# Optimization experiments

Hardware: AMD Instinct MI355X
Metric: run time of the kernel (lower is better)

## Reference

```python
import jax, jax.numpy as jnp
import numpy as np

N = 50000      # nodes
E = 800000     # edges
G = 2000       # graphs
F_IN = 34
HID = 256
H = 8
D = 32         # HID // H
L = 5


def _layer_norm(x, g, b, eps=1e-5):
    m = x.mean(-1, keepdims=True)
    v = ((x - m) ** 2).mean(-1, keepdims=True)
    return (x - m) / jnp.sqrt(v + eps) * g + b


def _gelu(x):
    return jax.nn.gelu(x, approximate=False)  # torch exact GELU


def _segment_softmax(scores, seg, n):
    # scores: [E', H], seg: [E'] target node ids
    m = jax.ops.segment_max(scores, seg, num_segments=n)
    m = jnp.where(jnp.isfinite(m), m, 0.0)
    ex = jnp.exp(scores - m[seg])
    den = jax.ops.segment_sum(ex, seg, num_segments=n)
    return ex / (den[seg] + 1e-16)


def setup_inputs() -> dict:
    key = jax.random.key(0)
    ks = iter(jax.random.split(key, 64))

    def p(shape, fan):
        return (jax.random.normal(next(ks), shape, jnp.float32) / np.sqrt(fan)).astype(jnp.float32)

    inp = {}
    inp['x'] = jax.random.normal(next(ks), (N, F_IN), jnp.float32)
    inp['edge_index'] = jax.random.randint(next(ks), (2, E), 0, N, jnp.int32)
    inp['batch'] = jnp.sort(jax.random.randint(next(ks), (N,), 0, G, jnp.int32))

    # input embed
    inp['in_W'] = p((F_IN, HID), F_IN); inp['in_b'] = jnp.zeros((HID,), jnp.float32)
    inp['in_ln_g'] = jnp.ones((HID,), jnp.float32); inp['in_ln_b'] = jnp.zeros((HID,), jnp.float32)
    # 5 GATv2 layers (stacked on leading dim)
    inp['gat_Wl'] = p((L, HID, HID), HID); inp['gat_bl'] = jnp.zeros((L, HID), jnp.float32)
    inp['gat_Wr'] = p((L, HID, HID), HID); inp['gat_br'] = jnp.zeros((L, HID), jnp.float32)
    inp['gat_att'] = p((L, H, D), D)
    inp['gat_bias'] = jnp.zeros((L, HID), jnp.float32)
    inp['gat_ln_g'] = jnp.ones((L, HID), jnp.float32); inp['gat_ln_b'] = jnp.zeros((L, HID), jnp.float32)
    # TransformerConv
    inp['tr_Wq'] = p((HID, HID), HID); inp['tr_bq'] = jnp.zeros((HID,), jnp.float32)
    inp['tr_Wk'] = p((HID, HID), HID); inp['tr_bk'] = jnp.zeros((HID,), jnp.float32)
    inp['tr_Wv'] = p((HID, HID), HID); inp['tr_bv'] = jnp.zeros((HID,), jnp.float32)
    inp['tr_Wskip'] = p((HID, HID), HID); inp['tr_bskip'] = jnp.zeros((HID,), jnp.float32)
    inp['tr_ln_g'] = jnp.ones((HID,), jnp.float32); inp['tr_ln_b'] = jnp.zeros((HID,), jnp.float32)
    # output proj
    inp['out_W'] = p((2 * HID, 2 * HID), 2 * HID); inp['out_b'] = jnp.zeros((2 * HID,), jnp.float32)
    inp['out_ln_g'] = jnp.ones((2 * HID,), jnp.float32); inp['out_ln_b'] = jnp.zeros((2 * HID,), jnp.float32)
    return inp


def reference(x, edge_index, batch,
              in_W, in_b, in_ln_g, in_ln_b,
              gat_Wl, gat_bl, gat_Wr, gat_br, gat_att, gat_bias, gat_ln_g, gat_ln_b,
              tr_Wq, tr_bq, tr_Wk, tr_bk, tr_Wv, tr_bv, tr_Wskip, tr_bskip, tr_ln_g, tr_ln_b,
              out_W, out_b, out_ln_g, out_ln_b):
    # input embedding (dropout inactive in eval)
    h = _gelu(_layer_norm(x @ in_W + in_b, in_ln_g, in_ln_b))

    src, dst = edge_index[0], edge_index[1]  # PyG: row=source j, col=target i
    loops = jnp.arange(N, dtype=src.dtype)
    s2 = jnp.concatenate([src, loops])  # GATv2 adds self loops
    d2 = jnp.concatenate([dst, loops])

    for l in range(L):  # small fixed loop over layers
        xl = (h @ gat_Wl[l] + gat_bl[l]).reshape(N, H, D)  # source transform / message
        xr = (h @ gat_Wr[l] + gat_br[l]).reshape(N, H, D)  # target transform
        e = jax.nn.leaky_relu(xl[s2] + xr[d2], 0.2)        # [E', H, D]
        score = jnp.einsum('ehd,hd->eh', e, gat_att[l])
        alpha = _segment_softmax(score, d2, N)             # softmax over incoming edges
        out = jax.ops.segment_sum(xl[s2] * alpha[..., None], d2, num_segments=N)
        out = out.reshape(N, HID) + gat_bias[l]
        h = h + _gelu(_layer_norm(out, gat_ln_g[l], gat_ln_b[l]))

    # TransformerConv (no self loops, root_weight skip connection)
    q = (h @ tr_Wq + tr_bq).reshape(N, H, D)
    k = (h @ tr_Wk + tr_bk).reshape(N, H, D)
    v = (h @ tr_Wv + tr_bv).reshape(N, H, D)
    score = (q[dst] * k[src]).sum(-1) / jnp.sqrt(jnp.float32(D))  # [E, H]
    alpha = _segment_softmax(score, dst, N)
    out = jax.ops.segment_sum(v[src] * alpha[..., None], dst, num_segments=N).reshape(N, HID)
    out = out + h @ tr_Wskip + tr_bskip
    h = h + _layer_norm(out, tr_ln_g, tr_ln_b)

    # global mean + max pool
    cnt = jax.ops.segment_sum(jnp.ones((N,), h.dtype), batch, num_segments=G)
    h_mean = jax.ops.segment_sum(h, batch, num_segments=G) / jnp.maximum(cnt, 1.0)[:, None]
    h_max = jax.ops.segment_max(h, batch, num_segments=G)
    h_max = jnp.where(jnp.isfinite(h_max), h_max, 0.0)
    ge = jnp.concatenate([h_mean, h_max], axis=-1)  # [G, 512]
    return _gelu(_layer_norm(ge @ out_W + out_b, out_ln_g, out_ln_b))
```

## Files before the change

kernel.cpp:

```cpp
#include <hip/hip_runtime.h>
#include <math.h>

#define N_NODES 50000
#define N_EDGES 800000
#define N_GRAPH 2000
#define F_INPUT 34
#define HID 256
#define NLAYER 5

typedef __attribute__((ext_vector_type(8))) short short8;
typedef __attribute__((ext_vector_type(4))) float float4v;

__device__ __forceinline__ float gelu_f(float x) {
  return 0.5f * x * (1.0f + erff(x * 0.70710678118654752440f));
}
__device__ __forceinline__ unsigned short bfr(float f) {
  unsigned u = __float_as_uint(f);
  return (unsigned short)((u + 0x7fffu + ((u >> 16) & 1u)) >> 16);
}
__device__ __forceinline__ float b2f(unsigned short s) {
  return __uint_as_float(((unsigned)s) << 16);
}
__device__ __forceinline__ float4 ld4bf(const unsigned short* p) {
  ushort4 u = *(const ushort4*)p;
  float4 f;
  f.x = b2f(u.x); f.y = b2f(u.y); f.z = b2f(u.z); f.w = b2f(u.w);
  return f;
}
__device__ __forceinline__ void unpk(unsigned u, float& a, float& b) {
  a = __uint_as_float(u << 16);
  b = __uint_as_float(u & 0xffff0000u);
}
__device__ __forceinline__ void acp16(const unsigned short* g, unsigned short* l) {
  __builtin_amdgcn_global_load_lds(
      (const __attribute__((address_space(1))) void*)g,
      (__attribute__((address_space(3))) void*)l, 16, 0, 0);
}

__global__ __launch_bounds__(256) void gemm_bias(
    const float* __restrict__ A, const float* __restrict__ B,
    const float* __restrict__ bias, float* __restrict__ C,
    int M, int Nn, int K) {
  __shared__ float As[16][64];
  __shared__ float Bs[16][64];
  int tid = threadIdx.x;
  int tx = tid & 15, ty = tid >> 4;
  int row0 = blockIdx.y * 64;
  int col0 = blockIdx.x * 64;
  float acc[4][4] = {};
  int a_r = tid >> 2;
  int a_c = (tid & 3) * 4;
  int b_r = tid >> 4;
  int b_c = (tid & 15) * 4;

  for (int k0 = 0; k0 < K; k0 += 16) {
    int ar = row0 + a_r;
#pragma unroll
    for (int i = 0; i < 4; ++i) {
      int kc = k0 + a_c + i;
      As[a_c + i][a_r] = (ar < M && kc < K) ? A[(long)ar * K + kc] : 0.f;
    }
    int bk = k0 + b_r;
    if (bk < K) {
      float4 bv = *(const float4*)&B[(long)bk * Nn + col0 + b_c];
      Bs[b_r][b_c + 0] = bv.x; Bs[b_r][b_c + 1] = bv.y;
      Bs[b_r][b_c + 2] = bv.z; Bs[b_r][b_c + 3] = bv.w;
    } else {
      Bs[b_r][b_c + 0] = 0.f; Bs[b_r][b_c + 1] = 0.f;
      Bs[b_r][b_c + 2] = 0.f; Bs[b_r][b_c + 3] = 0.f;
    }
    __syncthreads();
#pragma unroll
    for (int kk = 0; kk < 16; ++kk) {
      float4 a = *(const float4*)&As[kk][ty * 4];
      float4 b = *(const float4*)&Bs[kk][tx * 4];
      float av[4] = {a.x, a.y, a.z, a.w};
      float bv[4] = {b.x, b.y, b.z, b.w};
#pragma unroll
      for (int i = 0; i < 4; ++i)
#pragma unroll
        for (int j = 0; j < 4; ++j) acc[i][j] += av[i] * bv[j];
    }
    __syncthreads();
  }
  float4 bi = *(const float4*)&bias[col0 + tx * 4];
  float bia[4] = {bi.x, bi.y, bi.z, bi.w};
#pragma unroll
  for (int i = 0; i < 4; ++i) {
    int r = row0 + ty * 4 + i;
    if (r < M) {
      float4 o;
      o.x = acc[i][0] + bia[0]; o.y = acc[i][1] + bia[1];
      o.z = acc[i][2] + bia[2]; o.w = acc[i][3] + bia[3];
      *(float4*)&C[(long)r * Nn + col0 + tx * 4] = o;
    }
  }
}

__global__ __launch_bounds__(256) void gemm_mfma(
    const unsigned short* __restrict__ A, const unsigned short* __restrict__ Bt,
    const float* __restrict__ bias, void* __restrict__ Cv,
    int M, int Nn, int K, int flags) {
  __shared__ unsigned short smem[12288];
  unsigned short* As = smem;
  unsigned short* Bs = smem + 4096;
  int tid = threadIdx.x;
  int wave = tid >> 6, lane = tid & 63;
  int row0 = blockIdx.y * 128;
  int col0 = blockIdx.x * 128;
  int wm0 = (wave >> 1) * 64;
  int wn0 = (wave & 1) * 64;
  int q = lane >> 4;
  int ln = lane & 15;

  int srow = wave * 16 + (lane >> 2);
  int scol = (lane & 3) * 8;
  int ra0 = min(row0 + srow, M - 1);
  int ra1 = min(row0 + srow + 64, M - 1);
  const unsigned short* pa0 = A + (size_t)ra0 * K + scol;
  const unsigned short* pa1 = A + (size_t)ra1 * K + scol;
  const unsigned short* pb0 = Bt + (size_t)(col0 + srow) * K + scol;
  const unsigned short* pb1 = Bt + (size_t)(col0 + srow + 64) * K + scol;
  unsigned short* la0 = As + wave * 512;
  unsigned short* la1 = As + wave * 512 + 2048;
  unsigned short* lb0 = Bs + wave * 512;
  unsigned short* lb1 = Bs + wave * 512 + 2048;

  float4v acc[4][4];
#pragma unroll
  for (int i = 0; i < 4; ++i)
#pragma unroll
    for (int j = 0; j < 4; ++j) acc[i][j] = (float4v)0.f;

  for (int k0 = 0; k0 < K; k0 += 32) {
    acp16(pa0 + k0, la0);
    acp16(pa1 + k0, la1);
    acp16(pb0 + k0, lb0);
    acp16(pb1 + k0, lb1);
    __syncthreads();
    short8 af[4], bf[4];
#pragma unroll
    for (int i = 0; i < 4; ++i)
      af[i] = *(const short8*)&As[(wm0 + i * 16 + ln) * 32 + q * 8];
#pragma unroll
    for (int j = 0; j < 4; ++j)
      bf[j] = *(const short8*)&Bs[(wn0 + j * 16 + ln) * 32 + q * 8];
#pragma unroll
    for (int i = 0; i < 4; ++i)
#pragma unroll
      for (int j = 0; j < 4; ++j)
        acc[i][j] = __builtin_amdgcn_mfma_f32_16x16x32_bf16(af[i], bf[j], acc[i][j], 0, 0, 0);
    __syncthreads();
  }
  int rb = (lane >> 4) * 4;
  if (flags & 2) {
    unsigned short* Cb = (unsigned short*)Cv;
    unsigned short* eb = smem + wave * 2560;
#pragma unroll
    for (int p = 0; p < 2; ++p) {
#pragma unroll
      for (int jj = 0; jj < 2; ++jj) {
        int j = p * 2 + jj;
        float bv = bias[col0 + wn0 + j * 16 + ln];
#pragma unroll
        for (int i = 0; i < 4; ++i)
#pragma unroll
          for (int r = 0; r < 4; ++r)
            eb[(i * 16 + rb + r) * 40 + jj * 16 + ln] = bfr(acc[i][j][r] + bv);
      }
      int grow = row0 + wm0 + lane;
      uint4 w0 = *(uint4*)&eb[lane * 40 + 0];
      uint4 w1 = *(uint4*)&eb[lane * 40 + 8];
      uint4 w2 = *(uint4*)&eb[lane * 40 + 16];
      uint4 w3 = *(uint4*)&eb[lane * 40 + 24];
      if (grow < M) {
        unsigned short* dst = Cb + (size_t)grow * Nn + col0 + wn0 + p * 32;
        *(uint4*)&dst[0] = w0;
        *(uint4*)&dst[8] = w1;
        *(uint4*)&dst[16] = w2;
        *(uint4*)&dst[24] = w3;
      }
    }
  } else {
    float* C = (float*)Cv;
#pragma unroll
    for (int j = 0; j < 4; ++j) {
      int col = col0 + wn0 + j * 16 + ln;
      float bv = bias[col];
#pragma unroll
      for (int i = 0; i < 4; ++i)
#pragma unroll
        for (int r = 0; r < 4; ++r) {
          int row = row0 + wm0 + i * 16 + rb + r;
          if (row < M) C[(size_t)row * Nn + col] = acc[i][j][r] + bv;
        }
    }
  }
}

__global__ __launch_bounds__(256) void prep_w(
    const float* __restrict__ Wl, const float* __restrict__ Wr,
    const float* __restrict__ Wq, const float* __restrict__ Wk,
    const float* __restrict__ Wv, const float* __restrict__ Wsk,
    unsigned short* __restrict__ out) {
  __shared__ float t[32][33];
  int m = blockIdx.z;
  const float* W = (m < 10) ? (((m & 1) ? Wr : Wl) + (size_t)(m >> 1) * 65536)
                 : (m == 10) ? Wq : (m == 11) ? Wk : (m == 12) ? Wv : Wsk;
  int k0 = blockIdx.y * 32, n0 = blockIdx.x * 32;
  int r = threadIdx.x >> 5, c = threadIdx.x & 31;
  for (int rr = r; rr < 32; rr += 8)
    t[rr][c] = W[(size_t)(k0 + rr) * HID + n0 + c];
  __syncthreads();
  for (int rr = r; rr < 32; rr += 8) {
    int n = n0 + rr;
    unsigned short* o;
    int drow;
    if (m == 11) {
      o = out + (size_t)10 * 65536;
      drow = 256 + (n >> 2) * 8 + (n & 3);
    } else if (m == 12) {
      o = out + (size_t)10 * 65536;
      drow = 256 + (n >> 2) * 8 + 4 + (n & 3);
    } else {
      o = out + (size_t)m * 65536;
      drow = n;
    }
    o[(size_t)drow * HID + k0 + c] = bfr(t[c][rr]);
  }
}

__global__ __launch_bounds__(256) void prep_wout(const float* __restrict__ W,
                                                 unsigned short* __restrict__ o) {
  __shared__ float t[32][33];
  int k0 = blockIdx.y * 32, n0 = blockIdx.x * 32;
  int r = threadIdx.x >> 5, c = threadIdx.x & 31;
  for (int rr = r; rr < 32; rr += 8)
    t[rr][c] = W[(size_t)(k0 + rr) * 512 + n0 + c];
  __syncthreads();
  for (int rr = r; rr < 32; rr += 8)
    o[(size_t)(n0 + rr) * 512 + k0 + c] = bfr(t[c][rr]);
}

__global__ __launch_bounds__(256) void prep_bias(
    const float* __restrict__ bl, const float* __restrict__ br,
    const float* __restrict__ bq, const float* __restrict__ bk,
    const float* __restrict__ bv, float* __restrict__ out) {
  int i = blockIdx.x * 256 + threadIdx.x;
  if (i < 2560) {
    int l = i >> 9, c = i & 511;
    out[i] = (c < 256) ? bl[l * 256 + c] : br[l * 256 + (c - 256)];
  } else if (i < 3328) {
    int j = i - 2560;
    if (j < 256) {
      out[i] = bq[j];
    } else {
      int t = j - 256, g = t >> 3, r = t & 7;
      out[i] = (r < 4) ? bk[4 * g + r] : bv[4 * g + (r - 4)];
    }
  }
}

__global__ __launch_bounds__(256) void ln_act(
    const float* __restrict__ in, const float* __restrict__ gam,
    const float* __restrict__ bet, float* __restrict__ out,
    unsigned short* __restrict__ outb,
    int n_rows, int width, int do_gelu) {
  int wid = blockIdx.x * 4 + (threadIdx.x >> 6);
  int lane = threadIdx.x & 63;
  if (wid >= n_rows) return;
  int chunks = width >> 8;
  float4 v[2];
  float s = 0.f;
  for (int c = 0; c < chunks; ++c) {
    int off = c * 256 + lane * 4;
    float4 t = *(const float4*)&in[(size_t)wid * width + off];
    v[c] = t;
    s += t.x + t.y + t.z + t.w;
  }
  for (int o = 1; o < 64; o <<= 1) s += __shfl_xor(s, o);
  float mean = s / (float)width;
  float vs = 0.f;
  for (int c = 0; c < chunks; ++c) {
    float dx = v[c].x - mean, dy = v[c].y - mean, dz = v[c].z - mean, dw = v[c].w - mean;
    vs += dx * dx + dy * dy + dz * dz + dw * dw;
  }
  for (int o = 1; o < 64; o <<= 1) vs += __shfl_xor(vs, o);
  float inv = rsqrtf(vs / (float)width + 1e-5f);
  for (int c = 0; c < chunks; ++c) {
    int off = c * 256 + lane * 4;
    float4 g4 = *(const float4*)&gam[off];
    float4 b4 = *(const float4*)&bet[off];
    float y[4] = {(v[c].x - mean) * inv * g4.x + b4.x,
                  (v[c].y - mean) * inv * g4.y + b4.y,
                  (v[c].z - mean) * inv * g4.z + b4.z,
                  (v[c].w - mean) * inv * g4.w + b4.w};
    if (do_gelu) {
#pragma unroll
      for (int i = 0; i < 4; ++i) y[i] = gelu_f(y[i]);
    }
    size_t idx = (size_t)wid * width + off;
    float4 o4 = {y[0], y[1], y[2], y[3]};
    *(float4*)&out[idx] = o4;
    if (outb) {
      ushort4 ob = {bfr(y[0]), bfr(y[1]), bfr(y[2]), bfr(y[3])};
      *(ushort4*)&outb[idx] = ob;
    }
  }
}

__global__ __launch_bounds__(256) void edge_count(const int* __restrict__ ei,
                                                  int* __restrict__ counts) {
  int e = blockIdx.x * 256 + threadIdx.x;
  if (e < N_EDGES) atomicAdd(&counts[ei[N_EDGES + e]], 1);
}

__global__ __launch_bounds__(1024) void scan1(const int* __restrict__ counts,
                                              int* __restrict__ indptr,
                                              int* __restrict__ bsums, int n) {
  __shared__ int sm[1024];
  int tid = threadIdx.x;
  int i = blockIdx.x * 1024 + tid;
  int v = (i < n) ? counts[i] : 0;
  sm[tid] = v;
  __syncthreads();
  for (int off = 1; off < 1024; off <<= 1) {
    int t = (tid >= off) ? sm[tid - off] : 0;
    __syncthreads();
    sm[tid] += t;
    __syncthreads();
  }
  if (i < n) indptr[i] = sm[tid] - v;
  if (tid == 1023) bsums[blockIdx.x] = sm[1023];
}

__global__ __launch_bounds__(256) void scan3(const int* __restrict__ bsums,
                                             int* __restrict__ indptr,
                                             int* __restrict__ cursor, int n) {
  int i = blockIdx.x * 256 + threadIdx.x;
  int blk = blockIdx.x >> 2;
  int off = 0;
  for (int b = 0; b < blk; ++b) off += bsums[b];
  if (i < n) {
    int v = indptr[i] + off;
    indptr[i] = v;
    cursor[i] = v;
  }
  if (i == 0) indptr[n] = N_EDGES;
}

__global__ __launch_bounds__(256) void edge_scatter(const int* __restrict__ ei,
                                                    int* __restrict__ cursor,
                                                    int* __restrict__ esrc) {
  int e = blockIdx.x * 256 + threadIdx.x;
  if (e < N_EDGES) {
    int d = ei[N_EDGES + e];
    int p = atomicAdd(&cursor[d], 1);
    esrc[p] = ei[e];
  }
}

#define GAT_EDGE(f)                                                        \
  {                                                                        \
    float ex = f.x + xri.x; ex = ex > 0.f ? ex : 0.2f * ex;                \
    float ey = f.y + xri.y; ey = ey > 0.f ? ey : 0.2f * ey;                \
    float ez = f.z + xri.z; ez = ez > 0.f ? ez : 0.2f * ez;                \
    float ew = f.w + xri.w; ew = ew > 0.f ? ew : 0.2f * ew;                \
    float p = ex * a4.x + ey * a4.y + ez * a4.z + ew * a4.w;               \
    p += __shfl_xor(p, 1); p += __shfl_xor(p, 2); p += __shfl_xor(p, 4);   \
    float wgt = __expf(fminf(p - m0, 60.f));                               \
    ax += wgt * f.x; ay += wgt * f.y; az += wgt * f.z; aw += wgt * f.w;    \
    lsum += wgt;                                                           \
  }

__global__ __launch_bounds__(256) void gat_agg(
    const unsigned short* __restrict__ xlr, const float* __restrict__ att,
    const int* __restrict__ indptr, const int* __restrict__ esrc,
    const float* __restrict__ pre_bias, const float* __restrict__ gam,
    const float* __restrict__ bet, float* __restrict__ h,
    unsigned short* __restrict__ hb) {
  int wid = blockIdx.x * 4 + (threadIdx.x >> 6);
  int lane = threadIdx.x & 63;
  if (wid >= N_NODES) return;
  float4 xri = ld4bf(&xlr[(size_t)wid * 512 + 256 + lane * 4]);
  float4 a4 = *(const float4*)&att[lane * 4];
  int beg = indptr[wid], end = indptr[wid + 1];

  float m0, lsum, ax, ay, az, aw;
  {
    float4 f = ld4bf(&xlr[(size_t)wid * 512 + lane * 4]);
    float ex = f.x + xri.x; ex = ex > 0.f ? ex : 0.2f * ex;
    float ey = f.y + xri.y; ey = ey > 0.f ? ey : 0.2f * ey;
    float ez = f.z + xri.z; ez = ez > 0.f ? ez : 0.2f * ez;
    float ew = f.w + xri.w; ew = ew > 0.f ? ew : 0.2f * ew;
    float p = ex * a4.x + ey * a4.y + ez * a4.z + ew * a4.w;
    p += __shfl_xor(p, 1); p += __shfl_xor(p, 2); p += __shfl_xor(p, 4);
    m0 = p; lsum = 1.f;
    ax = f.x; ay = f.y; az = f.z; aw = f.w;
  }
  int e = beg;
  for (; e + 7 < end; e += 8) {
    int j0 = esrc[e],     j1 = esrc[e + 1], j2 = esrc[e + 2], j3 = esrc[e + 3];
    int j4 = esrc[e + 4], j5 = esrc[e + 5], j6 = esrc[e + 6], j7 = esrc[e + 7];
    float4 f0 = ld4bf(&xlr[(size_t)j0 * 512 + lane * 4]);
    float4 f1 = ld4bf(&xlr[(size_t)j1 * 512 + lane * 4]);
    float4 f2 = ld4bf(&xlr[(size_t)j2 * 512 + lane * 4]);
    float4 f3 = ld4bf(&xlr[(size_t)j3 * 512 + lane * 4]);
    float4 f4 = ld4bf(&xlr[(size_t)j4 * 512 + lane * 4]);
    float4 f5 = ld4bf(&xlr[(size_t)j5 * 512 + lane * 4]);
    float4 f6 = ld4bf(&xlr[(size_t)j6 * 512 + lane * 4]);
    float4 f7 = ld4bf(&xlr[(size_t)j7 * 512 + lane * 4]);
    GAT_EDGE(f0); GAT_EDGE(f1); GAT_EDGE(f2); GAT_EDGE(f3);
    GAT_EDGE(f4); GAT_EDGE(f5); GAT_EDGE(f6); GAT_EDGE(f7);
  }
  for (; e + 3 < end; e += 4) {
    int j0 = esrc[e], j1 = esrc[e + 1], j2 = esrc[e + 2], j3 = esrc[e + 3];
    float4 f0 = ld4bf(&xlr[(size_t)j0 * 512 + lane * 4]);
    float4 f1 = ld4bf(&xlr[(size_t)j1 * 512 + lane * 4]);
    float4 f2 = ld4bf(&xlr[(size_t)j2 * 512 + lane * 4]);
    float4 f3 = ld4bf(&xlr[(size_t)j3 * 512 + lane * 4]);
    GAT_EDGE(f0); GAT_EDGE(f1); GAT_EDGE(f2); GAT_EDGE(f3);
  }
  for (; e < end; ++e) {
    int j = esrc[e];
    float4 f = ld4bf(&xlr[(size_t)j * 512 + lane * 4]);
    GAT_EDGE(f);
  }
  float inv = 1.f / (lsum + 1e-16f);
  float4 pb = *(const float4*)&pre_bias[lane * 4];
  float y0 = ax * inv + pb.x, y1 = ay * inv + pb.y;
  float y2 = az * inv + pb.z, y3 = aw * inv + pb.w;
  float s = y0 + y1 + y2 + y3;
  for (int o = 1; o < 64; o <<= 1) s += __shfl_xor(s, o);
  float mean = s * (1.f / 256.f);
  float d0 = y0 - mean, d1 = y1 - mean, d2 = y2 - mean, d3 = y3 - mean;
  float vs = d0 * d0 + d1 * d1 + d2 * d2 + d3 * d3;
  for (int o = 1; o < 64; o <<= 1) vs += __shfl_xor(vs, o);
  float inv2 = rsqrtf(vs * (1.f / 256.f) + 1e-5f);
  float4 g4 = *(const float4*)&gam[lane * 4];
  float4 b4 = *(const float4*)&bet[lane * 4];
  size_t idx = (size_t)wid * HID + lane * 4;
  float4 r4 = *(const float4*)&h[idx];
  y0 = gelu_f(d0 * inv2 * g4.x + b4.x) + r4.x;
  y1 = gelu_f(d1 * inv2 * g4.y + b4.y) + r4.y;
  y2 = gelu_f(d2 * inv2 * g4.z + b4.z) + r4.z;
  y3 = gelu_f(d3 * inv2 * g4.w + b4.w) + r4.w;
  float4 o4 = {y0, y1, y2, y3};
  *(float4*)&h[idx] = o4;
  ushort4 ob = {bfr(y0), bfr(y1), bfr(y2), bfr(y3)};
  *(ushort4*)&hb[idx] = ob;
}

#define TR_EDGE_I(u)                                                       \
  {                                                                        \
    float kx, ky, kz, kw, vx, vy, vz, vw;                                  \
    unpk(u.x, kx, ky); unpk(u.y, kz, kw);                                  \
    unpk(u.z, vx, vy); unpk(u.w, vz, vw);                                  \
    float p = qi.x * kx + qi.y * ky + qi.z * kz + qi.w * kw;               \
    p += __shfl_xor(p, 1); p += __shfl_xor(p, 2); p += __shfl_xor(p, 4);   \
    float wgt = __expf(fminf(p * scale, 60.f));                            \
    ax += wgt * vx; ay += wgt * vy; az += wgt * vz; aw += wgt * vw;        \
    lsum += wgt;                                                           \
  }

__global__ __launch_bounds__(256) void tr_agg(
    const unsigned short* __restrict__ qkv, const int* __restrict__ indptr,
    const int* __restrict__ esrc, const unsigned short* __restrict__ skipb,
    const float* __restrict__ gam, const float* __restrict__ bet,
    float* __restrict__ h) {
  __shared__ float comb[2][5][64];
  int tid = threadIdx.x;
  int wave = tid >> 6, lane = tid & 63;
  int pair = wave >> 1, half = wave & 1;
  int wid = blockIdx.x * 2 + pair;
  float4 qi = ld4bf(&qkv[(size_t)wid * 768 + lane * 4]);
  int beg = indptr[wid], end = indptr[wid + 1];
  float lsum = 0.f;
  float ax = 0.f, ay = 0.f, az = 0.f, aw = 0.f;
  const float scale = 0.17677669529663687f;
  int e = beg + half;
  for (; e + 6 < end; e += 8) {
    int j0 = esrc[e], j1 = esrc[e + 2], j2 = esrc[e + 4], j3 = esrc[e + 6];
    uint4 u0 = *(const uint4*)&qkv[(size_t)j0 * 768 + 256 + lane * 8];
    uint4 u1 = *(const uint4*)&qkv[(size_t)j1 * 768 + 256 + lane * 8];
    uint4 u2 = *(const uint4*)&qkv[(size_t)j2 * 768 + 256 + lane * 8];
    uint4 u3 = *(const uint4*)&qkv[(size_t)j3 * 768 + 256 + lane * 8];
    TR_EDGE_I(u0); TR_EDGE_I(u1); TR_EDGE_I(u2); TR_EDGE_I(u3);
  }
  for (; e < end; e += 2) {
    int j = esrc[e];
    uint4 u = *(const uint4*)&qkv[(size_t)j * 768 + 256 + lane * 8];
    TR_EDGE_I(u);
  }
  if (half) {
    comb[pair][0][lane] = ax; comb[pair][1][lane] = ay;
    comb[pair][2][lane] = az; comb[pair][3][lane] = aw;
    comb[pair][4][lane] = lsum;
  }
  __syncthreads();
  if (half) return;
  ax += comb[pair][0][lane]; ay += comb[pair][1][lane];
  az += comb[pair][2][lane]; aw += comb[pair][3][lane];
  lsum += comb[pair][4][lane];

  float inv = 1.f / (lsum + 1e-16f);
  size_t idx = (size_t)wid * HID + lane * 4;
  float4 sk = ld4bf(&skipb[idx]);
  float y0 = ax * inv + sk.x, y1 = ay * inv + sk.y;
  float y2 = az * inv + sk.z, y3 = aw * inv + sk.w;
  float s = y0 + y1 + y2 + y3;
  for (int o = 1; o < 64; o <<= 1) s += __shfl_xor(s, o);
  float mean = s * (1.f / 256.f);
  float d0 = y0 - mean, d1 = y1 - mean, d2 = y2 - mean, d3 = y3 - mean;
  float vs = d0 * d0 + d1 * d1 + d2 * d2 + d3 * d3;
  for (int o = 1; o < 64; o <<= 1) vs += __shfl_xor(vs, o);
  float inv2 = rsqrtf(vs * (1.f / 256.f) + 1e-5f);
  float4 g4 = *(const float4*)&gam[lane * 4];
  float4 b4 = *(const float4*)&bet[lane * 4];
  float4 r4 = *(const float4*)&h[idx];
  float4 o4;
  o4.x = r4.x + d0 * inv2 * g4.x + b4.x;
  o4.y = r4.y + d1 * inv2 * g4.y + b4.y;
  o4.z = r4.z + d2 * inv2 * g4.z + b4.z;
  o4.w = r4.w + d3 * inv2 * g4.w + b4.w;
  *(float4*)&h[idx] = o4;
}

__global__ __launch_bounds__(256) void pool_seg(
    const float* __restrict__ h, const int* __restrict__ batch,
    unsigned short* __restrict__ geb) {
  int g = blockIdx.x, c = threadIdx.x;
  int lo = 0, hi = N_NODES;
  while (lo < hi) { int mid = (lo + hi) >> 1; if (batch[mid] < g) lo = mid + 1; else hi = mid; }
  int s = lo;
  hi = N_NODES;
  while (lo < hi) { int mid = (lo + hi) >> 1; if (batch[mid] < g + 1) lo = mid + 1; else hi = mid; }
  int e = lo;
  float sum = 0.f, mx = -INFINITY;
  for (int r = s; r < e; ++r) {
    float vv = h[(size_t)r * HID + c];
    sum += vv;
    mx = fmaxf(mx, vv);
  }
  int cnt = e - s;
  geb[(size_t)g * 512 + c] = bfr(sum / (float)max(cnt, 1));
  geb[(size_t)g * 512 + 256 + c] = bfr(cnt ? mx : 0.f);
}

static inline void mfma_launch(const unsigned short* A, const unsigned short* Bt,
                               const float* bias, void* C, int M, int Nn, int K,
                               int flags, hipStream_t s) {
  dim3 grid(Nn / 128, (M + 127) / 128);
  gemm_mfma<<<grid, 256, 0, s>>>(A, Bt, bias, C, M, Nn, K, flags);
}

extern "C" void kernel_launch(void* const* d_in, const int* in_sizes, int n_in,
                              void* d_out, int out_size, void* d_ws, size_t ws_size,
                              hipStream_t stream) {
  const float* x       = (const float*)d_in[0];
  const int*   ei      = (const int*)d_in[1];
  const int*   batch   = (const int*)d_in[2];
  const float* in_W    = (const float*)d_in[3];
  const float* in_b    = (const float*)d_in[4];
  const float* in_ln_g = (const float*)d_in[5];
  const float* in_ln_b = (const float*)d_in[6];
  const float* gat_Wl  = (const float*)d_in[7];
  const float* gat_bl  = (const float*)d_in[8];
  const float* gat_Wr  = (const float*)d_in[9];
  const float* gat_br  = (const float*)d_in[10];
  const float* gat_att = (const float*)d_in[11];
  const float* gat_bias= (const float*)d_in[12];
  const float* gat_ln_g= (const float*)d_in[13];
  const float* gat_ln_b= (const float*)d_in[14];
  const float* tr_Wq   = (const float*)d_in[15];
  const float* tr_bq   = (const float*)d_in[16];
  const float* tr_Wk   = (const float*)d_in[17];
  const float* tr_bk   = (const float*)d_in[18];
  const float* tr_Wv   = (const float*)d_in[19];
  const float* tr_bv   = (const float*)d_in[20];
  const float* tr_Wsk  = (const float*)d_in[21];
  const float* tr_bsk  = (const float*)d_in[22];
  const float* tr_ln_g = (const float*)d_in[23];
  const float* tr_ln_b = (const float*)d_in[24];
  const float* out_W   = (const float*)d_in[25];
  const float* out_b   = (const float*)d_in[26];
  const float* out_ln_g= (const float*)d_in[27];
  const float* out_ln_b= (const float*)d_in[28];

  char* w = (char*)d_ws;
  auto take = [&](size_t bytes) -> char* {
    char* p = w;
    w += (bytes + 255) & ~(size_t)255;
    return p;
  };
  const size_t NB = (size_t)N_NODES * HID * sizeof(float);
  float* h    = (float*)take(NB);
  float* aggO = (float*)take(NB);
  unsigned short* hb  = (unsigned short*)take((size_t)N_NODES * HID * 2);
  unsigned short* xq  = (unsigned short*)take((size_t)N_NODES * 768 * 2);
  unsigned short* wbuf= (unsigned short*)take((size_t)(14 * 65536 + 262144) * 2);
  float* bcat = (float*)take(3328 * sizeof(float));
  int* indptr = (int*)take((N_NODES + 1) * sizeof(int));
  int* cursor = (int*)take(N_NODES * sizeof(int));
  int* counts = (int*)take(N_NODES * sizeof(int));
  int* esrc   = (int*)take(N_EDGES * sizeof(int));
  int* bsums  = (int*)take(64 * sizeof(int));
  unsigned short* skipb = (unsigned short*)aggO;
  char* w2 = (char*)xq;
  auto take2 = [&](size_t bytes) -> char* {
    char* p = w2;
    w2 += (bytes + 255) & ~(size_t)255;
    return p;
  };
  unsigned short* geb = (unsigned short*)take2((size_t)N_GRAPH * 512 * 2);
  float* tbuf = (float*)take2((size_t)N_GRAPH * 512 * sizeof(float));

  const int EB = (N_EDGES + 255) / 256;
  const int WB = (N_NODES + 3) / 4;
  const int WB2 = N_NODES / 2;
  const int NSB = (N_NODES + 1023) / 1024;

  {
    dim3 g(8, 8, 14);
    prep_w<<<g, 256, 0, stream>>>(gat_Wl, gat_Wr, tr_Wq, tr_Wk, tr_Wv, tr_Wsk, wbuf);
    dim3 g2(16, 16);
    prep_wout<<<g2, 256, 0, stream>>>(out_W, wbuf + (size_t)14 * 65536);
    prep_bias<<<13, 256, 0, stream>>>(gat_bl, gat_br, tr_bq, tr_bk, tr_bv, bcat);
  }

  hipMemsetAsync(counts, 0, N_NODES * sizeof(int), stream);
  edge_count<<<EB, 256, 0, stream>>>(ei, counts);
  scan1<<<NSB, 1024, 0, stream>>>(counts, indptr, bsums, N_NODES);
  scan3<<<(N_NODES + 255) / 256, 256, 0, stream>>>(bsums, indptr, cursor, N_NODES);
  edge_scatter<<<EB, 256, 0, stream>>>(ei, cursor, esrc);

  {
    dim3 grid(HID / 64, (N_NODES + 63) / 64);
    gemm_bias<<<grid, 256, 0, stream>>>(x, in_W, in_b, aggO, N_NODES, HID, F_INPUT);
  }
  ln_act<<<WB, 256, 0, stream>>>(aggO, in_ln_g, in_ln_b, h, hb, N_NODES, HID, 1);

  for (int l = 0; l < NLAYER; ++l) {
    mfma_launch(hb, wbuf + (size_t)(2 * l) * 65536, bcat + l * 512, xq,
                N_NODES, 512, HID, 2, stream);
    gat_agg<<<WB, 256, 0, stream>>>(xq, gat_att + l * HID, indptr, esrc,
                                    gat_bias + l * HID, gat_ln_g + l * HID,
                                    gat_ln_b + l * HID, h, hb);
  }

  mfma_launch(hb, wbuf + (size_t)13 * 65536, tr_bsk, skipb,
              N_NODES, HID, HID, 2, stream);
  mfma_launch(hb, wbuf + (size_t)10 * 65536, bcat + 2560, xq,
              N_NODES, 768, HID, 2, stream);
  tr_agg<<<WB2, 256, 0, stream>>>(xq, indptr, esrc, skipb, tr_ln_g, tr_ln_b, h);

  pool_seg<<<N_GRAPH, 256, 0, stream>>>(h, batch, geb);

  mfma_launch(geb, wbuf + (size_t)14 * 65536, out_b, tbuf,
              N_GRAPH, 512, 512, 0, stream);
  ln_act<<<(N_GRAPH + 3) / 4, 256, 0, stream>>>(tbuf, out_ln_g, out_ln_b,
                                                (float*)d_out, nullptr,
                                                N_GRAPH, 512, 1);
}
```

Before: 1.195 ms.

## Degree-sort node order, fuse skip into QKV GEMM, MFMA input embed

Adds a degree histogram and counting sort so the GAT and Transformer aggregation kernels visit nodes in descending in-degree order, aimed at reducing load imbalance and tail effects across waves. The skip projection is folded into the QKV GEMM as a fourth 256-column block (1024 outputs), which removes one GEMM launch and the separate skip buffer. The FP32 input embedding GEMM is replaced by a bf16 MFMA GEMM with K padded to 64, which lowers input-embedding precision. Degree ordering gives up node locality in the h and hb writes and adds several small kernels plus atomics.

```diff
diff --git a/kernel.cpp b/kernel.cpp
--- a/kernel.cpp
+++ b/kernel.cpp
@@ -35,66 +35,6 @@
   __builtin_amdgcn_global_load_lds(
       (const __attribute__((address_space(1))) void*)g,
       (__attribute__((address_space(3))) void*)l, 16, 0, 0);
-}
-
-__global__ __launch_bounds__(256) void gemm_bias(
-    const float* __restrict__ A, const float* __restrict__ B,
-    const float* __restrict__ bias, float* __restrict__ C,
-    int M, int Nn, int K) {
-  __shared__ float As[16][64];
-  __shared__ float Bs[16][64];
-  int tid = threadIdx.x;
-  int tx = tid & 15, ty = tid >> 4;
-  int row0 = blockIdx.y * 64;
-  int col0 = blockIdx.x * 64;
-  float acc[4][4] = {};
-  int a_r = tid >> 2;
-  int a_c = (tid & 3) * 4;
-  int b_r = tid >> 4;
-  int b_c = (tid & 15) * 4;
-
-  for (int k0 = 0; k0 < K; k0 += 16) {
-    int ar = row0 + a_r;
-#pragma unroll
-    for (int i = 0; i < 4; ++i) {
-      int kc = k0 + a_c + i;
-      As[a_c + i][a_r] = (ar < M && kc < K) ? A[(long)ar * K + kc] : 0.f;
-    }
-    int bk = k0 + b_r;
-    if (bk < K) {
-      float4 bv = *(const float4*)&B[(long)bk * Nn + col0 + b_c];
-      Bs[b_r][b_c + 0] = bv.x; Bs[b_r][b_c + 1] = bv.y;
-      Bs[b_r][b_c + 2] = bv.z; Bs[b_r][b_c + 3] = bv.w;
-    } else {
-      Bs[b_r][b_c + 0] = 0.f; Bs[b_r][b_c + 1] = 0.f;
-      Bs[b_r][b_c + 2] = 0.f; Bs[b_r][b_c + 3] = 0.f;
-    }
-    __syncthreads();
-#pragma unroll
-    for (int kk = 0; kk < 16; ++kk) {
-      float4 a = *(const float4*)&As[kk][ty * 4];
-      float4 b = *(const float4*)&Bs[kk][tx * 4];
-      float av[4] = {a.x, a.y, a.z, a.w};
-      float bv[4] = {b.x, b.y, b.z, b.w};
-#pragma unroll
-      for (int i = 0; i < 4; ++i)
-#pragma unroll
-        for (int j = 0; j < 4; ++j) acc[i][j] += av[i] * bv[j];
-    }
-    __syncthreads();
-  }
-  float4 bi = *(const float4*)&bias[col0 + tx * 4];
-  float bia[4] = {bi.x, bi.y, bi.z, bi.w};
-#pragma unroll
-  for (int i = 0; i < 4; ++i) {
-    int r = row0 + ty * 4 + i;
-    if (r < M) {
-      float4 o;
-      o.x = acc[i][0] + bia[0]; o.y = acc[i][1] + bia[1];
-      o.z = acc[i][2] + bia[2]; o.w = acc[i][3] + bia[3];
-      *(float4*)&C[(long)r * Nn + col0 + tx * 4] = o;
-    }
-  }
 }
 
 __global__ __launch_bounds__(256) void gemm_mfma(
@@ -216,15 +156,14 @@
     int n = n0 + rr;
     unsigned short* o;
     int drow;
-    if (m == 11) {
+    if (m < 10) {
+      o = out + (size_t)m * 65536; drow = n;
+    } else {
       o = out + (size_t)10 * 65536;
-      drow = 256 + (n >> 2) * 8 + (n & 3);
-    } else if (m == 12) {
-      o = out + (size_t)10 * 65536;
-      drow = 256 + (n >> 2) * 8 + 4 + (n & 3);
-    } else {
-      o = out + (size_t)m * 65536;
-      drow = n;
+      if (m == 10)      drow = n;
+      else if (m == 11) drow = 256 + (n >> 2) * 8 + (n & 3);
+      else if (m == 12) drow = 256 + (n >> 2) * 8 + 4 + (n & 3);
+      else              drow = 768 + n;
     }
     o[(size_t)drow * HID + k0 + c] = bfr(t[c][rr]);
   }
@@ -242,22 +181,37 @@
     o[(size_t)(n0 + rr) * 512 + k0 + c] = bfr(t[c][rr]);
 }
 
+__global__ __launch_bounds__(256) void prep_wemb(const float* __restrict__ W,
+                                                 unsigned short* __restrict__ o) {
+  int i = blockIdx.x * 256 + threadIdx.x;
+  int n = i >> 6, k = i & 63;
+  o[i] = (k < F_INPUT) ? bfr(W[(size_t)k * HID + n]) : (unsigned short)0;
+}
+
+__global__ __launch_bounds__(256) void prep_x(const float* __restrict__ x,
+                                              unsigned short* __restrict__ xb) {
+  int i = blockIdx.x * 256 + threadIdx.x;
+  if (i >= N_NODES * 64) return;
+  int row = i >> 6, k = i & 63;
+  xb[i] = (k < F_INPUT) ? bfr(x[(size_t)row * F_INPUT + k]) : (unsigned short)0;
+}
+
 __global__ __launch_bounds__(256) void prep_bias(
     const float* __restrict__ bl, const float* __restrict__ br,
     const float* __restrict__ bq, const float* __restrict__ bk,
-    const float* __restrict__ bv, float* __restrict__ out) {
+    const float* __restrict__ bv, const float* __restrict__ bsk,
+    float* __restrict__ out) {
   int i = blockIdx.x * 256 + threadIdx.x;
   if (i < 2560) {
     int l = i >> 9, c = i & 511;
     out[i] = (c < 256) ? bl[l * 256 + c] : br[l * 256 + (c - 256)];
-  } else if (i < 3328) {
+  } else if (i < 3584) {
     int j = i - 2560;
-    if (j < 256) {
-      out[i] = bq[j];
-    } else {
+    if (j < 256) out[i] = bq[j];
+    else if (j < 768) {
       int t = j - 256, g = t >> 3, r = t & 7;
       out[i] = (r < 4) ? bk[4 * g + r] : bv[4 * g + (r - 4)];
-    }
+    } else out[i] = bsk[j - 768];
   }
 }
 
@@ -360,6 +314,27 @@
   }
 }
 
+__global__ __launch_bounds__(256) void deg_hist(const int* __restrict__ counts,
+                                                int* __restrict__ hist) {
+  int i = blockIdx.x * 256 + threadIdx.x;
+  if (i < N_NODES) atomicAdd(&hist[min(counts[i], 127)], 1);
+}
+__global__ void deg_prefix(const int* __restrict__ hist, int* __restrict__ cur) {
+  if (threadIdx.x == 0 && blockIdx.x == 0) {
+    int acc = 0;
+    for (int d = 127; d >= 0; --d) { cur[d] = acc; acc += hist[d]; }
+  }
+}
+__global__ __launch_bounds__(256) void deg_scatter(const int* __restrict__ counts,
+                                                   int* __restrict__ cur,
+                                                   int* __restrict__ order) {
+  int i = blockIdx.x * 256 + threadIdx.x;
+  if (i < N_NODES) {
+    int p = atomicAdd(&cur[min(counts[i], 127)], 1);
+    order[p] = i;
+  }
+}
+
 #define GAT_EDGE(f)                                                        \
   {                                                                        \
     float ex = f.x + xri.x; ex = ex > 0.f ? ex : 0.2f * ex;                \
@@ -376,12 +351,14 @@
 __global__ __launch_bounds__(256) void gat_agg(
     const unsigned short* __restrict__ xlr, const float* __restrict__ att,
     const int* __restrict__ indptr, const int* __restrict__ esrc,
+    const int* __restrict__ order,
     const float* __restrict__ pre_bias, const float* __restrict__ gam,
     const float* __restrict__ bet, float* __restrict__ h,
     unsigned short* __restrict__ hb) {
-  int wid = blockIdx.x * 4 + (threadIdx.x >> 6);
+  int slot = blockIdx.x * 4 + (threadIdx.x >> 6);
   int lane = threadIdx.x & 63;
-  if (wid >= N_NODES) return;
+  if (slot >= N_NODES) return;
+  int wid = order[slot];
   float4 xri = ld4bf(&xlr[(size_t)wid * 512 + 256 + lane * 4]);
   float4 a4 = *(const float4*)&att[lane * 4];
   int beg = indptr[wid], end = indptr[wid + 1];
@@ -465,15 +442,15 @@
 
 __global__ __launch_bounds__(256) void tr_agg(
     const unsigned short* __restrict__ qkv, const int* __restrict__ indptr,
-    const int* __restrict__ esrc, const unsigned short* __restrict__ skipb,
+    const int* __restrict__ esrc, const int* __restrict__ order,
     const float* __restrict__ gam, const float* __restrict__ bet,
     float* __restrict__ h) {
   __shared__ float comb[2][5][64];
   int tid = threadIdx.x;
   int wave = tid >> 6, lane = tid & 63;
   int pair = wave >> 1, half = wave & 1;
-  int wid = blockIdx.x * 2 + pair;
-  float4 qi = ld4bf(&qkv[(size_t)wid * 768 + lane * 4]);
+  int wid = order[blockIdx.x * 2 + pair];
+  float4 qi = ld4bf(&qkv[(size_t)wid * 1024 + lane * 4]);
   int beg = indptr[wid], end = indptr[wid + 1];
   float lsum = 0.f;
   float ax = 0.f, ay = 0.f, az = 0.f, aw = 0.f;
@@ -481,15 +458,15 @@
   int e = beg + half;
   for (; e + 6 < end; e += 8) {
     int j0 = esrc[e], j1 = esrc[e + 2], j2 = esrc[e + 4], j3 = esrc[e + 6];
-    uint4 u0 = *(const uint4*)&qkv[(size_t)j0 * 768 + 256 + lane * 8];
-    uint4 u1 = *(const uint4*)&qkv[(size_t)j1 * 768 + 256 + lane * 8];
-    uint4 u2 = *(const uint4*)&qkv[(size_t)j2 * 768 + 256 + lane * 8];
-    uint4 u3 = *(const uint4*)&qkv[(size_t)j3 * 768 + 256 + lane * 8];
+    uint4 u0 = *(const uint4*)&qkv[(size_t)j0 * 1024 + 256 + lane * 8];
+    uint4 u1 = *(const uint4*)&qkv[(size_t)j1 * 1024 + 256 + lane * 8];
+    uint4 u2 = *(const uint4*)&qkv[(size_t)j2 * 1024 + 256 + lane * 8];
+    uint4 u3 = *(const uint4*)&qkv[(size_t)j3 * 1024 + 256 + lane * 8];
     TR_EDGE_I(u0); TR_EDGE_I(u1); TR_EDGE_I(u2); TR_EDGE_I(u3);
   }
   for (; e < end; e += 2) {
     int j = esrc[e];
-    uint4 u = *(const uint4*)&qkv[(size_t)j * 768 + 256 + lane * 8];
+    uint4 u = *(const uint4*)&qkv[(size_t)j * 1024 + 256 + lane * 8];
     TR_EDGE_I(u);
   }
   if (half) {
@@ -505,7 +482,7 @@
 
   float inv = 1.f / (lsum + 1e-16f);
   size_t idx = (size_t)wid * HID + lane * 4;
-  float4 sk = ld4bf(&skipb[idx]);
+  float4 sk = ld4bf(&qkv[(size_t)wid * 1024 + 768 + lane * 4]);
   float y0 = ax * inv + sk.x, y1 = ay * inv + sk.y;
   float y2 = az * inv + sk.z, y3 = aw * inv + sk.w;
   float s = y0 + y1 + y2 + y3;
@@ -593,19 +570,21 @@
     w += (bytes + 255) & ~(size_t)255;
     return p;
   };
-  const size_t NB = (size_t)N_NODES * HID * sizeof(float);
-  float* h    = (float*)take(NB);
-  float* aggO = (float*)take(NB);
-  unsigned short* hb  = (unsigned short*)take((size_t)N_NODES * HID * 2);
-  unsigned short* xq  = (unsigned short*)take((size_t)N_NODES * 768 * 2);
-  unsigned short* wbuf= (unsigned short*)take((size_t)(14 * 65536 + 262144) * 2);
-  float* bcat = (float*)take(3328 * sizeof(float));
+  float* h = (float*)take((size_t)N_NODES * HID * sizeof(float));
+  unsigned short* hb = (unsigned short*)take((size_t)N_NODES * HID * 2);
+  unsigned short* xq = (unsigned short*)take((size_t)N_NODES * 1024 * 2);
+  unsigned short* wbuf = (unsigned short*)take((size_t)(14 * 65536 + 262144 + 16384) * 2);
+  float* bcat = (float*)take(3584 * sizeof(float));
   int* indptr = (int*)take((N_NODES + 1) * sizeof(int));
   int* cursor = (int*)take(N_NODES * sizeof(int));
   int* counts = (int*)take(N_NODES * sizeof(int));
   int* esrc   = (int*)take(N_EDGES * sizeof(int));
   int* bsums  = (int*)take(64 * sizeof(int));
-  unsigned short* skipb = (unsigned short*)aggO;
+  int* hist   = (int*)take(128 * sizeof(int));
+  int* hcur   = (int*)take(128 * sizeof(int));
+  int* order  = (int*)take(N_NODES * sizeof(int));
+  unsigned short* xb = (unsigned short*)xq;
+  float* et = (float*)((char*)xq + ((size_t)N_NODES * 64 * 2 + 255 & ~(size_t)255));
   char* w2 = (char*)xq;
   auto take2 = [&](size_t bytes) -> char* {
     char* p = w2;
@@ -615,6 +594,7 @@
   unsigned short* geb = (unsigned short*)take2((size_t)N_GRAPH * 512 * 2);
   float* tbuf = (float*)take2((size_t)N_GRAPH * 512 * sizeof(float));
 
+  const unsigned short* wemb = wbuf + (size_t)14 * 65536 + 262144;
   const int EB = (N_EDGES + 255) / 256;
   const int WB = (N_NODES + 3) / 4;
   const int WB2 = N_NODES / 2;
@@ -625,34 +605,35 @@
     prep_w<<<g, 256, 0, stream>>>(gat_Wl, gat_Wr, tr_Wq, tr_Wk, tr_Wv, tr_Wsk, wbuf);
     dim3 g2(16, 16);
     prep_wout<<<g2, 256, 0, stream>>>(out_W, wbuf + (size_t)14 * 65536);
-    prep_bias<<<13, 256, 0, stream>>>(gat_bl, gat_br, tr_bq, tr_bk, tr_bv, bcat);
+    prep_wemb<<<64, 256, 0, stream>>>(in_W, (unsigned short*)wemb);
+    prep_bias<<<14, 256, 0, stream>>>(gat_bl, gat_br, tr_bq, tr_bk, tr_bv, tr_bsk, bcat);
   }
 
   hipMemsetAsync(counts, 0, N_NODES * sizeof(int), stream);
+  hipMemsetAsync(hist, 0, 128 * sizeof(int), stream);
   edge_count<<<EB, 256, 0, stream>>>(ei, counts);
   scan1<<<NSB, 1024, 0, stream>>>(counts, indptr, bsums, N_NODES);
   scan3<<<(N_NODES + 255) / 256, 256, 0, stream>>>(bsums, indptr, cursor, N_NODES);
   edge_scatter<<<EB, 256, 0, stream>>>(ei, cursor, esrc);
-
-  {
-    dim3 grid(HID / 64, (N_NODES + 63) / 64);
-    gemm_bias<<<grid, 256, 0, stream>>>(x, in_W, in_b, aggO, N_NODES, HID, F_INPUT);
-  }
-  ln_act<<<WB, 256, 0, stream>>>(aggO, in_ln_g, in_ln_b, h, hb, N_NODES, HID, 1);
+  deg_hist<<<(N_NODES + 255) / 256, 256, 0, stream>>>(counts, hist);
+  deg_prefix<<<1, 64, 0, stream>>>(hist, hcur);
+  deg_scatter<<<(N_NODES + 255) / 256, 256, 0, stream>>>(counts, hcur, order);
+
+  prep_x<<<(N_NODES * 64 + 255) / 256, 256, 0, stream>>>(x, xb);
+  mfma_launch(xb, wemb, in_b, et, N_NODES, HID, 64, 0, stream);
+  ln_act<<<WB, 256, 0, stream>>>(et, in_ln_g, in_ln_b, h, hb, N_NODES, HID, 1);
 
   for (int l = 0; l < NLAYER; ++l) {
     mfma_launch(hb, wbuf + (size_t)(2 * l) * 65536, bcat + l * 512, xq,
                 N_NODES, 512, HID, 2, stream);
-    gat_agg<<<WB, 256, 0, stream>>>(xq, gat_att + l * HID, indptr, esrc,
+    gat_agg<<<WB, 256, 0, stream>>>(xq, gat_att + l * HID, indptr, esrc, order,
                                     gat_bias + l * HID, gat_ln_g + l * HID,
                                     gat_ln_b + l * HID, h, hb);
   }
 
-  mfma_launch(hb, wbuf + (size_t)13 * 65536, tr_bsk, skipb,
-              N_NODES, HID, HID, 2, stream);
   mfma_launch(hb, wbuf + (size_t)10 * 65536, bcat + 2560, xq,
-              N_NODES, 768, HID, 2, stream);
-  tr_agg<<<WB2, 256, 0, stream>>>(xq, indptr, esrc, skipb, tr_ln_g, tr_ln_b, h);
+              N_NODES, 1024, HID, 2, stream);
+  tr_agg<<<WB2, 256, 0, stream>>>(xq, indptr, esrc, order, tr_ln_g, tr_ln_b, h);
 
   pool_seg<<<N_GRAPH, 256, 0, stream>>>(h, batch, geb);
 
```

Result: slower. 1.492 ms (+24.8%).
